# Kernel tuning notes

Hardware: AMD Instinct MI355X
Metric: run time of the kernel (lower is better)

## Reference

```python
import jax, jax.numpy as jnp
import numpy as np

# Model constants (match init_kwargs config)
D_MODEL, D_INNER, D_HEAD, N_HEADS = 1024, 2048, 64, 32
D_STATE, D_CONV, CHUNK, N_LAYERS = 64, 4, 256, 2
CONV_DIM = D_INNER + 2 * D_STATE        # n_groups = 1
D_IN_PROJ = 2 * D_INNER + 2 * D_STATE + N_HEADS
B_SZ, L_SEQ = 2, 4096
EPS = 1e-5


def setup_inputs() -> dict:
    key = jax.random.key(0)
    ks = jax.random.split(key, 8)
    x = jax.random.normal(ks[0], (B_SZ, L_SEQ, D_MODEL), jnp.float32)
    in_proj_w = jax.random.normal(ks[1], (N_LAYERS, D_IN_PROJ, D_MODEL), jnp.float32) * 0.02
    conv_w = jax.random.normal(ks[2], (N_LAYERS, CONV_DIM, D_CONV), jnp.float32) * 0.2
    conv_b = jax.random.normal(ks[3], (N_LAYERS, CONV_DIM), jnp.float32) * 0.02
    # dt_bias init as in the torch code: inverse-softplus of dt ~ LogUniform(1e-3, 1e-1)
    dt = jnp.exp(jax.random.uniform(ks[4], (N_LAYERS, N_HEADS))
                 * (np.log(0.1) - np.log(0.001)) + np.log(0.001))
    dt = jnp.clip(dt, 1e-4, None)
    dt_bias = dt + jnp.log(-jnp.expm1(-dt))
    A_log = jnp.log(jax.random.uniform(ks[5], (N_LAYERS, N_HEADS), minval=1.0, maxval=16.0))
    D = jnp.ones((N_LAYERS, N_HEADS), jnp.float32)
    gnorm_w = jnp.ones((N_LAYERS, D_INNER), jnp.float32)
    out_proj_w = jax.random.normal(ks[6], (N_LAYERS, D_MODEL, D_INNER), jnp.float32) * 0.02
    norm_w = jnp.ones((N_LAYERS, D_MODEL), jnp.float32)
    return dict(x=x, in_proj_w=in_proj_w, conv_w=conv_w, conv_b=conv_b, dt_bias=dt_bias,
                A_log=A_log, D=D, gnorm_w=gnorm_w, out_proj_w=out_proj_w, norm_w=norm_w)


def _rmsnorm(x, w, eps=EPS):
    return x * jax.lax.rsqrt(jnp.mean(x * x, axis=-1, keepdims=True) + eps) * w


def _segsum(x):
    # x: (..., T) -> (..., T, T) with S[i, j] = sum_{j < k <= i} x[k], -inf above diag
    T = x.shape[-1]
    cs = jnp.cumsum(x, axis=-1)
    d = cs[..., :, None] - cs[..., None, :]
    return jnp.where(jnp.tril(jnp.ones((T, T), bool)), d, -jnp.inf)


def _causal_conv1d(x, w, b):
    # depthwise causal conv: x (B,L,C), w (C,K), b (C)
    K = w.shape[-1]
    L = x.shape[1]
    xp = jnp.pad(x, ((0, 0), (K - 1, 0), (0, 0)))
    out = jnp.broadcast_to(b, x.shape)
    for i in range(K):
        out = out + xp[:, i:i + L, :] * w[:, i]
    return out


def _ssd(X, dt, A, B, C, D):
    # Exact chunked SSD scan (mamba_chunk_scan_combined), n_groups=1.
    # X (b,l,h,p), dt (b,l,h), A (h), B,C (b,l,n)
    b, l, h, p = X.shape
    n = B.shape[-1]
    nc = l // CHUNK
    Xdt = X * dt[..., None]
    dA = (dt * A).reshape(b, nc, CHUNK, h).transpose(0, 3, 1, 2)     # (b,h,z,c)
    dAcs = jnp.cumsum(dA, axis=-1)
    Lmat = jnp.exp(_segsum(dA))                                      # (b,h,z,c,c)
    Bc = B.reshape(b, nc, CHUNK, n)
    Cc = C.reshape(b, nc, CHUNK, n)
    Xc = Xdt.reshape(b, nc, CHUNK, h, p)
    # intra-chunk (diagonal) part
    G = jnp.einsum('bzln,bzsn->bzls', Cc, Bc)                        # (b,z,c,c)
    M = G[:, None] * Lmat                                            # (b,h,z,c,c)
    Yd = jnp.einsum('bhzls,bzshp->bzlhp', M, Xc)
    # chunk states
    decay_states = jnp.exp(dAcs[..., -1:] - dAcs)                    # (b,h,z,c)
    states = jnp.einsum('bzln,bhzl,bzlhp->bzhpn', Bc, decay_states, Xc)
    # inter-chunk recurrence
    chunk_decay = jnp.exp(_segsum(jnp.pad(dAcs[..., -1], ((0, 0), (0, 0), (1, 0)))))
    states0 = jnp.concatenate([jnp.zeros_like(states[:, :1]), states], axis=1)
    prev = jnp.einsum('bhzc,bchpn->bzhpn', chunk_decay, states0)[:, :-1]
    Yo = jnp.einsum('bzln,bzhpn,bhzl->bzlhp', Cc, prev, jnp.exp(dAcs))
    Y = (Yd + Yo).reshape(b, l, h, p) + X * D[None, None, :, None]
    return Y


def _block(x, in_w, cw, cb, dtb, a_log, d_skip, gw, ow, nw):
    b, l, _ = x.shape
    h = _rmsnorm(x, nw)
    zxbcdt = jnp.einsum('bld,ed->ble', h, in_w)
    z = zxbcdt[..., :D_INNER]
    xBC = zxbcdt[..., D_INNER:D_INNER + CONV_DIM]
    dt = jax.nn.softplus(zxbcdt[..., D_INNER + CONV_DIM:] + dtb)      # (b,l,H)
    xBC = jax.nn.silu(_causal_conv1d(xBC, cw, cb))
    xs = xBC[..., :D_INNER].reshape(b, l, N_HEADS, D_HEAD)
    Bm = xBC[..., D_INNER:D_INNER + D_STATE]
    Cm = xBC[..., D_INNER + D_STATE:]
    A = -jnp.exp(a_log)
    y = _ssd(xs, dt, A, Bm, Cm, d_skip).reshape(b, l, D_INNER)
    y = _rmsnorm(y * jax.nn.silu(z), gw)                              # gated RMSNorm (gate before norm)
    return x + jnp.einsum('bli,di->bld', y, ow)


def reference(x, in_proj_w, conv_w, conv_b, dt_bias, A_log, D, gnorm_w, out_proj_w, norm_w):
    for i in range(in_proj_w.shape[0]):
        x = _block(x, in_proj_w[i], conv_w[i], conv_b[i], dt_bias[i],
                   A_log[i], D[i], gnorm_w[i], out_proj_w[i], norm_w[i])
    return x
```

## Files before the change

### kernel.cpp

```cpp
#include <hip/hip_runtime.h>

#define DMODEL   1024
#define DINNER   2048
#define NHEADS   32
#define DHEAD    64
#define DSTATE   64
#define CONVDIM  2176
#define DINPROJ  4256
#define LSEQ     4096
#define BSZ      2
#define NCHUNK   16
#define CHUNK    256
#define NROWS    8192
#define NPAD     4352
#define XT_P     264
#define M_P      40

typedef __attribute__((ext_vector_type(8))) short  short8;
typedef __attribute__((ext_vector_type(4))) float  f32x4;
typedef __attribute__((ext_vector_type(4))) unsigned short us4;

__device__ __forceinline__ float bf2f(unsigned short u){
  return __uint_as_float(((unsigned int)u) << 16);
}
__device__ __forceinline__ unsigned short f2bf(float f){
  unsigned int i = __float_as_uint(f);
  i += 0x7fffu + ((i >> 16) & 1u);
  return (unsigned short)(i >> 16);
}

__device__ __forceinline__ void gl_lds16(const void* g, void* l){
  __builtin_amdgcn_global_load_lds(
      (const __attribute__((address_space(1))) unsigned int*)g,
      (__attribute__((address_space(3))) unsigned int*)l, 16, 0, 0);
}

__global__ void cast_pad_kernel(const float* __restrict__ src, unsigned short* __restrict__ dst,
                                int rows_src, int cols, long long total){
  long long i = (long long)blockIdx.x * 256 + threadIdx.x;
  if (i >= total) return;
  long long r = i / cols;
  dst[i] = (r < rows_src) ? f2bf(src[i]) : (unsigned short)0;
}

__global__ void rmsnorm_kernel(const float* __restrict__ x, const float* __restrict__ w,
                               unsigned short* __restrict__ out){
  int r = blockIdx.x, t = threadIdx.x;
  const float* xr = x + (size_t)r * DMODEL;
  float v[4]; float s = 0.f;
#pragma unroll
  for (int i = 0; i < 4; ++i){ v[i] = xr[t + i*256]; s += v[i]*v[i]; }
  __shared__ float red[4];
  for (int off = 32; off; off >>= 1) s += __shfl_down(s, off, 64);
  if ((t & 63) == 0) red[t >> 6] = s;
  __syncthreads();
  s = red[0] + red[1] + red[2] + red[3];
  float sc = rsqrtf(s * (1.f/DMODEL) + 1e-5f);
#pragma unroll
  for (int i = 0; i < 4; ++i)
    out[(size_t)r*DMODEL + t + i*256] = f2bf(v[i]*sc*w[t + i*256]);
}

template<int EPI>
__launch_bounds__(256, 3)
__global__ void gemm_bt(const unsigned short* __restrict__ A, const unsigned short* __restrict__ Bw,
                        void* __restrict__ Cout, const float* __restrict__ Cres,
                        int K, int Nstore){
  __shared__ __align__(16) unsigned short As[128*64];
  __shared__ __align__(16) unsigned short Bs[128*64];
  const int m0 = blockIdx.y * 128, n0 = blockIdx.x * 128;
  const int t = threadIdx.x, w = t >> 6, lane = t & 63;
  const int wr = w >> 1, wc = w & 1;
  const int srow = lane >> 3;
  const int scol = (lane & 7) * 8;
  f32x4 acc[4][4] = {};

  for (int k0 = 0; k0 < K; k0 += 64){
#pragma unroll
    for (int it = 0; it < 4; ++it){
      int rr = (w*4 + it)*8 + srow;
      gl_lds16(A  + (size_t)(m0 + rr)*K + k0 + scol, &As[(w*4 + it)*512]);
      gl_lds16(Bw + (size_t)(n0 + rr)*K + k0 + scol, &Bs[(w*4 + it)*512]);
    }
    __syncthreads();
#pragma unroll
    for (int kk = 0; kk < 64; kk += 32){
      short8 af[4], bfr[4];
      int col = kk + (lane >> 4)*8;
#pragma unroll
      for (int m = 0; m < 4; ++m)
        af[m] = *(const short8*)&As[(wr*64 + m*16 + (lane & 15))*64 + col];
#pragma unroll
      for (int n = 0; n < 4; ++n)
        bfr[n] = *(const short8*)&Bs[(wc*64 + n*16 + (lane & 15))*64 + col];
#pragma unroll
      for (int m = 0; m < 4; ++m)
#pragma unroll
        for (int n = 0; n < 4; ++n)
          acc[m][n] = __builtin_amdgcn_mfma_f32_16x16x32_bf16(af[m], bfr[n], acc[m][n], 0, 0, 0);
    }
    __syncthreads();
  }

#pragma unroll
  for (int m = 0; m < 4; ++m){
#pragma unroll
    for (int n = 0; n < 4; ++n){
      int col = n0 + wc*64 + n*16 + (lane & 15);
      if (col < Nstore){
#pragma unroll
        for (int r = 0; r < 4; ++r){
          int row = m0 + wr*64 + m*16 + (lane >> 4)*4 + r;
          if (EPI == 0)
            ((unsigned short*)Cout)[(size_t)row*Nstore + col] = f2bf(acc[m][n][r]);
          else
            ((float*)Cout)[(size_t)row*Nstore + col] =
                Cres[(size_t)row*Nstore + col] + acc[m][n][r];
        }
      }
    }
  }
}

__global__ void conv_silu_kernel(const unsigned short* __restrict__ zx,
                                 const float* __restrict__ cw, const float* __restrict__ cb,
                                 unsigned short* __restrict__ X, unsigned short* __restrict__ Bm,
                                 unsigned short* __restrict__ Cm){
  int gid = blockIdx.x*256 + threadIdx.x;
  if (gid >= (CONVDIM/8)*(NROWS/64)) return;
  const int oc = gid % (CONVDIM/8);
  const int rb = gid / (CONVDIM/8);
  const int c = oc*8;
  const size_t r0 = (size_t)rb*64;
  const int l0 = (int)(r0 & (LSEQ-1));
  float w[4][8], bias[8];
#pragma unroll
  for (int j = 0; j < 8; ++j){
    bias[j] = cb[c+j];
#pragma unroll
    for (int i = 0; i < 4; ++i) w[i][j] = cw[(c+j)*4 + i];
  }
  const unsigned short* src = zx + DINNER + c;
  float p[3][8];
#pragma unroll
  for (int i = 0; i < 3; ++i){
    if (l0 - 3 + i >= 0){
      short8 v = *(const short8*)(src + (r0 - 3 + i)*DINPROJ);
#pragma unroll
      for (int j = 0; j < 8; ++j) p[i][j] = bf2f((unsigned short)v[j]);
    } else {
#pragma unroll
      for (int j = 0; j < 8; ++j) p[i][j] = 0.f;
    }
  }
  for (int it = 0; it < 64; ++it){
    const size_t r = r0 + it;
    short8 v = *(const short8*)(src + r*DINPROJ);
    float cur[8];
    short8 ov;
#pragma unroll
    for (int j = 0; j < 8; ++j){
      cur[j] = bf2f((unsigned short)v[j]);
      float a = bias[j] + w[0][j]*p[0][j] + w[1][j]*p[1][j] + w[2][j]*p[2][j] + w[3][j]*cur[j];
      float s = a / (1.f + __expf(-a));
      ov[j] = (short)f2bf(s);
    }
    if (c < DINNER)             *(short8*)(X  + r*DINNER + c) = ov;
    else if (c < DINNER+DSTATE) *(short8*)(Bm + r*DSTATE + (c-DINNER)) = ov;
    else                        *(short8*)(Cm + r*DSTATE + (c-DINNER-DSTATE)) = ov;
#pragma unroll
    for (int j = 0; j < 8; ++j){ p[0][j]=p[1][j]; p[1][j]=p[2][j]; p[2][j]=cur[j]; }
  }
}

__global__ void dtscan_kernel(const unsigned short* __restrict__ zx, const float* __restrict__ dtb,
                              const float* __restrict__ A_log,
                              float* __restrict__ dt_sp, float* __restrict__ dAcs_g){
  const int z = blockIdx.x, hh = blockIdx.y, b = blockIdx.z;
  const int t = threadIdx.x;
  __shared__ float sdA[CHUNK];
  const float Ah = -__expf(A_log[hh]);
  size_t r = (size_t)b*LSEQ + z*CHUNK + t;
  float raw = bf2f(zx[r*DINPROJ + DINNER + CONVDIM + hh]) + dtb[hh];
  float dtv = raw > 20.f ? raw : log1pf(__expf(raw));
  sdA[t] = dtv * Ah;
  __syncthreads();
  for (int off = 1; off < CHUNK; off <<= 1){
    float v = (t >= off) ? sdA[t - off] : 0.f;
    __syncthreads();
    sdA[t] += v;
    __syncthreads();
  }
  size_t hb = (size_t)(b*NHEADS + hh);
  dt_sp[hb*LSEQ + z*CHUNK + t] = dtv;
  dAcs_g[(hb*NCHUNK + z)*CHUNK + t] = sdA[t];
}

__launch_bounds__(256, 2)
__global__ void chunk_main_kernel(const unsigned short* __restrict__ X,
                                  const unsigned short* __restrict__ Bm,
                                  const unsigned short* __restrict__ Cm,
                                  const float* __restrict__ dt_sp,
                                  const float* __restrict__ dAcs_g,
                                  float* __restrict__ states,
                                  unsigned short* __restrict__ Yb){
  const int z = blockIdx.x, hh = blockIdx.y, b = blockIdx.z;
  const int t = threadIdx.x, w = t >> 6, lane = t & 63;
  __shared__ __align__(16) unsigned short Xt[64 * XT_P];
  __shared__ __align__(16) unsigned short U[64 * XT_P];
  __shared__ float sdA[CHUNK];
  __shared__ float sdt[CHUNK];

  const size_t row0 = (size_t)b*LSEQ + z*CHUNK;
  const size_t hb = (size_t)(b*NHEADS + hh);
  sdA[t] = dAcs_g[(hb*NCHUNK + z)*CHUNK + t];
  sdt[t] = dt_sp[hb*LSEQ + z*CHUNK + t];
  __syncthreads();
  const float total = sdA[CHUNK-1];

  for (int it = 0; it < 16; ++it){
    int l = it*16 + (t >> 4);
    int p4 = (t & 15) * 4;
    float dtl = sdt[l];
    float dec = __expf(total - sdA[l]);
    us4 xv = *(const us4*)(X  + (row0 + l)*DINNER + hh*DHEAD + p4);
    us4 bv = *(const us4*)(Bm + (row0 + l)*DSTATE + p4);
#pragma unroll
    for (int j = 0; j < 4; ++j){
      Xt[(p4 + j)*XT_P + l] = f2bf(bf2f(xv[j]) * dtl);
      U [(p4 + j)*XT_P + l] = f2bf(bf2f(bv[j]) * dec);
    }
  }
  __syncthreads();

  {
    f32x4 sacc[4] = {};
    for (int k2 = 0; k2 < 8; ++k2){
      int kc = k2*32 + (lane >> 4)*8;
      short8 a = *(const short8*)&U[(w*16 + (lane & 15))*XT_P + kc];
#pragma unroll
      for (int pt = 0; pt < 4; ++pt){
        short8 bfr = *(const short8*)&Xt[(pt*16 + (lane & 15))*XT_P + kc];
        sacc[pt] = __builtin_amdgcn_mfma_f32_16x16x32_bf16(a, bfr, sacc[pt], 0, 0, 0);
      }
    }
    float* sp = states + (((size_t)b*NCHUNK + z)*NHEADS + hh)*(DHEAD*DSTATE);
#pragma unroll
    for (int pt = 0; pt < 4; ++pt){
      int p = pt*16 + (lane & 15);
#pragma unroll
      for (int r = 0; r < 4; ++r){
        int n = w*16 + (lane >> 4)*4 + r;
        sp[p*DSTATE + n] = sacc[pt][r];
      }
    }
  }
  __syncthreads();

  unsigned short* Mw = U + w * (64 * M_P);
  short8 cfr[4][2];
#pragma unroll
  for (int lt = 0; lt < 4; ++lt){
    int lg = w + lt*4;
#pragma unroll
    for (int k2 = 0; k2 < 2; ++k2)
      cfr[lt][k2] = *(const short8*)(Cm + (row0 + lg*16 + (lane & 15))*DSTATE + k2*32 + (lane >> 4)*8);
  }
  f32x4 yacc[4][4] = {};
  for (int st = 0; st < 8; ++st){
    short8 gb[2][2];
#pragma unroll
    for (int ss = 0; ss < 2; ++ss)
#pragma unroll
      for (int k2 = 0; k2 < 2; ++k2)
        gb[ss][k2] = *(const short8*)(Bm + (row0 + st*32 + ss*16 + (lane & 15))*DSTATE + k2*32 + (lane >> 4)*8);
    short8 xb[4];
#pragma unroll
    for (int pt = 0; pt < 4; ++pt)
      xb[pt] = *(const short8*)&Xt[(pt*16 + (lane & 15))*XT_P + st*32 + (lane >> 4)*8];
#pragma unroll
    for (int lt = 0; lt < 4; ++lt){
      int lg = w + lt*4;
      if (st*32 > lg*16 + 15) continue;
#pragma unroll
      for (int ss = 0; ss < 2; ++ss){
        f32x4 g = {};
        g = __builtin_amdgcn_mfma_f32_16x16x32_bf16(cfr[lt][0], gb[ss][0], g, 0, 0, 0);
        g = __builtin_amdgcn_mfma_f32_16x16x32_bf16(cfr[lt][1], gb[ss][1], g, 0, 0, 0);
        int s = st*32 + ss*16 + (lane & 15);
        float sdAs = sdA[s];
#pragma unroll
        for (int r = 0; r < 4; ++r){
          int l = lg*16 + (lane >> 4)*4 + r;
          float m = (s <= l) ? __expf(sdA[l] - sdAs) : 0.f;
          Mw[(lt*16 + (lane >> 4)*4 + r)*M_P + ss*16 + (lane & 15)] = f2bf(g[r] * m);
        }
      }
      short8 mf = *(const short8*)&Mw[(lt*16 + (lane & 15))*M_P + (lane >> 4)*8];
#pragma unroll
      for (int pt = 0; pt < 4; ++pt)
        yacc[lt][pt] = __builtin_amdgcn_mfma_f32_16x16x32_bf16(mf, xb[pt], yacc[lt][pt], 0, 0, 0);
    }
  }
  __syncthreads();

  unsigned short* Yst = U + w * 4096;
#pragma unroll
  for (int lt = 0; lt < 4; ++lt)
#pragma unroll
    for (int pt = 0; pt < 4; ++pt)
#pragma unroll
      for (int r = 0; r < 4; ++r){
        int row = lt*16 + (lane >> 4)*4 + r;
        int c = pt*16 + (lane & 15);
        int cs = (c & 7) | ((((c >> 3) ^ (row & 7)) & 7) << 3);
        Yst[row*64 + cs] = f2bf(yacc[lt][pt][r]);
      }
  __syncthreads();
  {
    int ltl = lane >> 4, rr = lane & 15;
    int row = ltl*16 + rr;
    int lg = (w + ltl*4)*16 + rr;
    unsigned short* dst = Yb + (row0 + lg)*DINNER + hh*DHEAD;
#pragma unroll
    for (int k = 0; k < 8; ++k){
      short8 v = *(const short8*)&Yst[row*64 + ((k ^ (row & 7)) << 3)];
      *(short8*)(dst + k*8) = v;
    }
  }
}

__launch_bounds__(256)
__global__ void state_recur_kernel(const float* __restrict__ states, const float* __restrict__ dAcs_g,
                                   unsigned short* __restrict__ prev_bf){
  const int hh = blockIdx.x, b = blockIdx.y, t = threadIdx.x;
  float S[16];
#pragma unroll
  for (int k = 0; k < 16; ++k) S[k] = 0.f;
  for (int z = 0; z < NCHUNK; ++z){
    size_t base = (((size_t)b*NCHUNK + z)*NHEADS + hh)*(DHEAD*DSTATE);
    float cd = __expf(dAcs_g[(((size_t)(b*NHEADS + hh))*NCHUNK + z)*CHUNK + CHUNK-1]);
#pragma unroll
    for (int k = 0; k < 16; ++k){
      size_t idx = base + (size_t)k*256 + t;
      float st = states[idx];
      prev_bf[idx] = f2bf(S[k]);
      S[k] = S[k]*cd + st;
    }
  }
}

__launch_bounds__(256, 4)
__global__ void chunk_out_kernel(const unsigned short* __restrict__ X,
                                 const unsigned short* __restrict__ Cm,
                                 const float* __restrict__ dAcs_g, const unsigned short* __restrict__ prev_bf,
                                 const float* __restrict__ Dp, unsigned short* __restrict__ Yb){
  const int z = blockIdx.x, hh = blockIdx.y, b = blockIdx.z;
  const int t = threadIdx.x, w = t >> 6, lane = t & 63;
  __shared__ __align__(16) unsigned short Yo[4][64*64];
  __shared__ float sdA[CHUNK];
  const size_t row0 = (size_t)b*LSEQ + z*CHUNK;
  sdA[t] = dAcs_g[(((size_t)(b*NHEADS + hh))*NCHUNK + z)*CHUNK + t];
  __syncthreads();
  const unsigned short* pvb = prev_bf + (((size_t)b*NCHUNK + z)*NHEADS + hh)*(DHEAD*DSTATE);
  const float Dh = Dp[hh];

  f32x4 acc[4][4] = {};
#pragma unroll
  for (int k2 = 0; k2 < 2; ++k2){
    int kc = k2*32 + (lane >> 4)*8;
    short8 a[4], bfr[4];
#pragma unroll
    for (int lt = 0; lt < 4; ++lt)
      a[lt] = *(const short8*)(Cm + (row0 + w*64 + lt*16 + (lane & 15))*DSTATE + kc);
#pragma unroll
    for (int pt = 0; pt < 4; ++pt)
      bfr[pt] = *(const short8*)(pvb + (size_t)(pt*16 + (lane & 15))*DSTATE + kc);
#pragma unroll
    for (int lt = 0; lt < 4; ++lt)
#pragma unroll
      for (int pt = 0; pt < 4; ++pt)
        acc[lt][pt] = __builtin_amdgcn_mfma_f32_16x16x32_bf16(a[lt], bfr[pt], acc[lt][pt], 0, 0, 0);
  }

#pragma unroll
  for (int lt = 0; lt < 4; ++lt){
    float eA[4];
#pragma unroll
    for (int r = 0; r < 4; ++r)
      eA[r] = __expf(sdA[w*64 + lt*16 + (lane >> 4)*4 + r]);
#pragma unroll
    for (int pt = 0; pt < 4; ++pt){
      int c = pt*16 + (lane & 15);
#pragma unroll
      for (int r = 0; r < 4; ++r){
        int row = lt*16 + (lane >> 4)*4 + r;
        int blk = ((c >> 2) ^ (row & 15)) & 15;
        Yo[w][row*64 + (c & 3) + (blk << 2)] = f2bf(acc[lt][pt][r] * eA[r]);
      }
    }
  }
  __syncthreads();
  {
    int l = w*64 + lane;
    const unsigned short* xr = X + (row0 + l)*DINNER + hh*DHEAD;
    unsigned short* yr = Yb + (row0 + l)*DINNER + hh*DHEAD;
#pragma unroll
    for (int k = 0; k < 16; ++k){
      us4 v = *(const us4*)&Yo[w][lane*64 + (((k ^ (lane & 15)) & 15) << 2)];
      us4 yb = *(const us4*)(yr + k*4);
      us4 xv = *(const us4*)(xr + k*4);
      us4 o;
#pragma unroll
      for (int j = 0; j < 4; ++j)
        o[j] = f2bf(bf2f(yb[j]) + bf2f(v[j]) + Dh*bf2f(xv[j]));
      *(us4*)(yr + k*4) = o;
    }
  }
}

__global__ void gated_rmsnorm_kernel(const unsigned short* __restrict__ Yb,
                                     const unsigned short* __restrict__ zx,
                                     const float* __restrict__ gw, unsigned short* __restrict__ out){
  int r = blockIdx.x, t = threadIdx.x;
  float vals[8]; float s = 0.f;
#pragma unroll
  for (int i = 0; i < 8; ++i){
    int c = t + i*256;
    float y  = bf2f(Yb[(size_t)r*DINNER + c]);
    float zv = bf2f(zx[(size_t)r*DINPROJ + c]);
    float g  = y * (zv / (1.f + __expf(-zv)));
    vals[i] = g; s += g*g;
  }
  __shared__ float red[4];
  for (int off = 32; off; off >>= 1) s += __shfl_down(s, off, 64);
  if ((t & 63) == 0) red[t >> 6] = s;
  __syncthreads();
  s = red[0] + red[1] + red[2] + red[3];
  float sc = rsqrtf(s * (1.f/DINNER) + 1e-5f);
#pragma unroll
  for (int i = 0; i < 8; ++i)
    out[(size_t)r*DINNER + t + i*256] = f2bf(vals[i]*sc*gw[t + i*256]);
}

extern "C" void kernel_launch(void* const* d_in, const int* in_sizes, int n_in,
                              void* d_out, int out_size, void* d_ws, size_t ws_size,
                              hipStream_t stream){
  const float* x      = (const float*)d_in[0];
  const float* in_w   = (const float*)d_in[1];
  const float* conv_w = (const float*)d_in[2];
  const float* conv_b = (const float*)d_in[3];
  const float* dt_b   = (const float*)d_in[4];
  const float* A_log  = (const float*)d_in[5];
  const float* Dp     = (const float*)d_in[6];
  const float* gnw    = (const float*)d_in[7];
  const float* out_w  = (const float*)d_in[8];
  const float* norm_w = (const float*)d_in[9];
  float* outp = (float*)d_out;

  const size_t NEEDED =
      (size_t)NROWS*DMODEL*2 + (size_t)NPAD*DMODEL*2 + (size_t)DMODEL*DINNER*2
    + (size_t)NROWS*DINPROJ*2 + (size_t)NROWS*DINNER*2  + (size_t)NROWS*DINNER*2
    + (size_t)NROWS*DSTATE*2*2 + (size_t)BSZ*NHEADS*LSEQ*4
    + (size_t)BSZ*NHEADS*NCHUNK*CHUNK*4
    + (size_t)BSZ*NCHUNK*NHEADS*DHEAD*DSTATE*4
    + (size_t)BSZ*NCHUNK*NHEADS*DHEAD*DSTATE*2
    + 40*256;
  if (ws_size < NEEDED) return;

  char* p = (char*)d_ws;
  auto alloc = [&](size_t n){ char* r = p; p += (n + 255) & ~(size_t)255; return (void*)r; };
  unsigned short* h    = (unsigned short*)alloc((size_t)NROWS*DMODEL*2);
  unsigned short* wA   = (unsigned short*)alloc((size_t)NPAD*DMODEL*2);
  unsigned short* wO   = (unsigned short*)alloc((size_t)DMODEL*DINNER*2);
  unsigned short* zx   = (unsigned short*)alloc((size_t)NROWS*DINPROJ*2);
  unsigned short* X    = (unsigned short*)alloc((size_t)NROWS*DINNER*2);
  unsigned short* Yb   = (unsigned short*)alloc((size_t)NROWS*DINNER*2);
  unsigned short* Bm   = (unsigned short*)alloc((size_t)NROWS*DSTATE*2);
  unsigned short* Cm   = (unsigned short*)alloc((size_t)NROWS*DSTATE*2);
  float* dtbuf  = (float*)alloc((size_t)BSZ*NHEADS*LSEQ*4);
  float* dAcs   = (float*)alloc((size_t)BSZ*NHEADS*NCHUNK*CHUNK*4);
  float* states = (float*)alloc((size_t)BSZ*NCHUNK*NHEADS*DHEAD*DSTATE*4);
  unsigned short* prev_bf = (unsigned short*)alloc((size_t)BSZ*NCHUNK*NHEADS*DHEAD*DSTATE*2);
  unsigned short* yn = X;

  for (int layer = 0; layer < 2; ++layer){
    const float* xprev = (layer == 0) ? x : outp;
    float* xnext = outp;

    cast_pad_kernel<<<(NPAD*DMODEL + 255)/256, 256, 0, stream>>>(
        in_w + (size_t)layer*DINPROJ*DMODEL, wA, DINPROJ, DMODEL, (long long)NPAD*DMODEL);
    rmsnorm_kernel<<<NROWS, 256, 0, stream>>>(xprev, norm_w + layer*DMODEL, h);
    gemm_bt<0><<<dim3(NPAD/128, NROWS/128), 256, 0, stream>>>(
        h, wA, (void*)zx, nullptr, DMODEL, DINPROJ);
    conv_silu_kernel<<<((CONVDIM/8)*(NROWS/64) + 255)/256, 256, 0, stream>>>(
        zx, conv_w + (size_t)layer*CONVDIM*4, conv_b + layer*CONVDIM, X, Bm, Cm);
    dtscan_kernel<<<dim3(NCHUNK, NHEADS, BSZ), 256, 0, stream>>>(
        zx, dt_b + layer*NHEADS, A_log + layer*NHEADS, dtbuf, dAcs);
    chunk_main_kernel<<<dim3(NCHUNK, NHEADS, BSZ), 256, 0, stream>>>(
        X, Bm, Cm, dtbuf, dAcs, states, Yb);
    state_recur_kernel<<<dim3(NHEADS, BSZ), 256, 0, stream>>>(states, dAcs, prev_bf);
    chunk_out_kernel<<<dim3(NCHUNK, NHEADS, BSZ), 256, 0, stream>>>(
        X, Cm, dAcs, prev_bf, Dp + layer*NHEADS, Yb);
    gated_rmsnorm_kernel<<<NROWS, 256, 0, stream>>>(Yb, zx, gnw + layer*DINNER, yn);
    cast_pad_kernel<<<(DMODEL*DINNER + 255)/256, 256, 0, stream>>>(
        out_w + (size_t)layer*DMODEL*DINNER, wO, DMODEL, DINNER, (long long)DMODEL*DINNER);
    gemm_bt<1><<<dim3(DMODEL/128, NROWS/128), 256, 0, stream>>>(
        yn, wO, (void*)xnext, xprev, DINNER, DMODEL);
  }
  (void)in_sizes; (void)n_in; (void)out_size;
}
```

Before: 732.6 us.

## Fuse chunk output with gated RMSNorm and remap GEMM blocks across XCDs

Merges the chunk-output kernel (C·prev state MFMA plus D skip) with the gated RMSNorm into one kernel. Each 512-thread block handles 16 rows across all heads, so the Yb intermediate is no longer written and read back, and one launch is removed. The GEMMs now use a 1D grid with an XCD-aware remap of block IDs, meant to improve L2 locality across the chiplets. In exchange, the fused kernel uses about 66KB of LDS per block and reloads prev_bf per 16-row slice, which increases redundant state reads.

```diff
diff --git a/kernel.cpp b/kernel.cpp
--- a/kernel.cpp
+++ b/kernel.cpp
@@ -65,10 +65,13 @@
 __launch_bounds__(256, 3)
 __global__ void gemm_bt(const unsigned short* __restrict__ A, const unsigned short* __restrict__ Bw,
                         void* __restrict__ Cout, const float* __restrict__ Cres,
-                        int K, int Nstore){
+                        int K, int Nstore, int nbx){
   __shared__ __align__(16) unsigned short As[128*64];
   __shared__ __align__(16) unsigned short Bs[128*64];
-  const int m0 = blockIdx.y * 128, n0 = blockIdx.x * 128;
+  int id = blockIdx.x;
+  const int nwg = gridDim.x;
+  if ((nwg & 7) == 0) id = (id & 7)*(nwg >> 3) + (id >> 3);
+  const int m0 = (id / nbx) * 128, n0 = (id % nbx) * 128;
   const int t = threadIdx.x, w = t >> 6, lane = t & 63;
   const int wr = w >> 1, wc = w & 1;
   const int srow = lane >> 3;
@@ -350,97 +353,103 @@
   }
 }
 
-__launch_bounds__(256, 4)
-__global__ void chunk_out_kernel(const unsigned short* __restrict__ X,
+__launch_bounds__(512, 2)
+__global__ void chunk_fin_kernel(const unsigned short* __restrict__ X,
                                  const unsigned short* __restrict__ Cm,
-                                 const float* __restrict__ dAcs_g, const unsigned short* __restrict__ prev_bf,
-                                 const float* __restrict__ Dp, unsigned short* __restrict__ Yb){
-  const int z = blockIdx.x, hh = blockIdx.y, b = blockIdx.z;
+                                 const unsigned short* __restrict__ zx,
+                                 const float* __restrict__ dAcs_g,
+                                 const unsigned short* __restrict__ prev_bf,
+                                 const float* __restrict__ Dp,
+                                 const unsigned short* __restrict__ Yb,
+                                 const float* __restrict__ gnw,
+                                 unsigned short* __restrict__ yn){
+  const int s = blockIdx.x;
+  const int b = blockIdx.y;
+  const int z = s >> 4, sl = s & 15;
   const int t = threadIdx.x, w = t >> 6, lane = t & 63;
-  __shared__ __align__(16) unsigned short Yo[4][64*64];
-  __shared__ float sdA[CHUNK];
-  const size_t row0 = (size_t)b*LSEQ + z*CHUNK;
-  sdA[t] = dAcs_g[(((size_t)(b*NHEADS + hh))*NCHUNK + z)*CHUNK + t];
-  __syncthreads();
-  const unsigned short* pvb = prev_bf + (((size_t)b*NCHUNK + z)*NHEADS + hh)*(DHEAD*DSTATE);
-  const float Dh = Dp[hh];
-
-  f32x4 acc[4][4] = {};
-#pragma unroll
-  for (int k2 = 0; k2 < 2; ++k2){
-    int kc = k2*32 + (lane >> 4)*8;
-    short8 a[4], bfr[4];
-#pragma unroll
-    for (int lt = 0; lt < 4; ++lt)
-      a[lt] = *(const short8*)(Cm + (row0 + w*64 + lt*16 + (lane & 15))*DSTATE + kc);
-#pragma unroll
-    for (int pt = 0; pt < 4; ++pt)
-      bfr[pt] = *(const short8*)(pvb + (size_t)(pt*16 + (lane & 15))*DSTATE + kc);
-#pragma unroll
-    for (int lt = 0; lt < 4; ++lt)
-#pragma unroll
-      for (int pt = 0; pt < 4; ++pt)
-        acc[lt][pt] = __builtin_amdgcn_mfma_f32_16x16x32_bf16(a[lt], bfr[pt], acc[lt][pt], 0, 0, 0);
-  }
-
-#pragma unroll
-  for (int lt = 0; lt < 4; ++lt){
-    float eA[4];
-#pragma unroll
-    for (int r = 0; r < 4; ++r)
-      eA[r] = __expf(sdA[w*64 + lt*16 + (lane >> 4)*4 + r]);
+  const size_t row0 = (size_t)b*LSEQ + z*CHUNK + sl*16;
+  __shared__ __align__(16) unsigned short Yg[16][2056];
+  __shared__ float seA[NHEADS][16];
+  __shared__ float sDp[NHEADS];
+
+  {
+    int hh = t >> 4, r = t & 15;
+    seA[hh][r] = __expf(dAcs_g[(((size_t)(b*NHEADS + hh))*NCHUNK + z)*CHUNK + sl*16 + r]);
+    if (t < NHEADS) sDp[t] = Dp[t];
+  }
+  __syncthreads();
+
+  short8 cf[2];
+#pragma unroll
+  for (int k2 = 0; k2 < 2; ++k2)
+    cf[k2] = *(const short8*)(Cm + (row0 + (lane & 15))*DSTATE + k2*32 + (lane >> 4)*8);
+
+  for (int hi = 0; hi < 4; ++hi){
+    int hh = w*4 + hi;
+    const unsigned short* pvb = prev_bf + (((size_t)b*NCHUNK + z)*NHEADS + hh)*(DHEAD*DSTATE);
+    f32x4 acc[4] = {};
+#pragma unroll
+    for (int k2 = 0; k2 < 2; ++k2){
+      int kc = k2*32 + (lane >> 4)*8;
+#pragma unroll
+      for (int pt = 0; pt < 4; ++pt){
+        short8 bv = *(const short8*)(pvb + (size_t)(pt*16 + (lane & 15))*DSTATE + kc);
+        acc[pt] = __builtin_amdgcn_mfma_f32_16x16x32_bf16(cf[k2], bv, acc[pt], 0, 0, 0);
+      }
+    }
 #pragma unroll
     for (int pt = 0; pt < 4; ++pt){
-      int c = pt*16 + (lane & 15);
+      int c = hh*DHEAD + pt*16 + (lane & 15);
 #pragma unroll
       for (int r = 0; r < 4; ++r){
-        int row = lt*16 + (lane >> 4)*4 + r;
-        int blk = ((c >> 2) ^ (row & 15)) & 15;
-        Yo[w][row*64 + (c & 3) + (blk << 2)] = f2bf(acc[lt][pt][r] * eA[r]);
-      }
-    }
-  }
-  __syncthreads();
-  {
-    int l = w*64 + lane;
-    const unsigned short* xr = X + (row0 + l)*DINNER + hh*DHEAD;
-    unsigned short* yr = Yb + (row0 + l)*DINNER + hh*DHEAD;
-#pragma unroll
-    for (int k = 0; k < 16; ++k){
-      us4 v = *(const us4*)&Yo[w][lane*64 + (((k ^ (lane & 15)) & 15) << 2)];
-      us4 yb = *(const us4*)(yr + k*4);
-      us4 xv = *(const us4*)(xr + k*4);
-      us4 o;
-#pragma unroll
-      for (int j = 0; j < 4; ++j)
-        o[j] = f2bf(bf2f(yb[j]) + bf2f(v[j]) + Dh*bf2f(xv[j]));
-      *(us4*)(yr + k*4) = o;
-    }
-  }
-}
-
-__global__ void gated_rmsnorm_kernel(const unsigned short* __restrict__ Yb,
-                                     const unsigned short* __restrict__ zx,
-                                     const float* __restrict__ gw, unsigned short* __restrict__ out){
-  int r = blockIdx.x, t = threadIdx.x;
-  float vals[8]; float s = 0.f;
-#pragma unroll
-  for (int i = 0; i < 8; ++i){
-    int c = t + i*256;
-    float y  = bf2f(Yb[(size_t)r*DINNER + c]);
-    float zv = bf2f(zx[(size_t)r*DINPROJ + c]);
-    float g  = y * (zv / (1.f + __expf(-zv)));
-    vals[i] = g; s += g*g;
-  }
-  __shared__ float red[4];
-  for (int off = 32; off; off >>= 1) s += __shfl_down(s, off, 64);
-  if ((t & 63) == 0) red[t >> 6] = s;
-  __syncthreads();
-  s = red[0] + red[1] + red[2] + red[3];
-  float sc = rsqrtf(s * (1.f/DINNER) + 1e-5f);
-#pragma unroll
-  for (int i = 0; i < 8; ++i)
-    out[(size_t)r*DINNER + t + i*256] = f2bf(vals[i]*sc*gw[t + i*256]);
+        int row = (lane >> 4)*4 + r;
+        Yg[row][c] = f2bf(acc[pt][r] * seA[hh][row]);
+      }
+    }
+  }
+  __syncthreads();
+
+  const int row = t >> 5, i = t & 31;
+  const size_t grow = row0 + row;
+  float ss = 0.f;
+#pragma unroll
+  for (int j = 0; j < 8; ++j){
+    int c0 = i*8 + j*256;
+    short8 yo = *(const short8*)&Yg[row][c0];
+    short8 yd = *(const short8*)(Yb + grow*DINNER + c0);
+    short8 xv = *(const short8*)(X  + grow*DINNER + c0);
+    short8 zv = *(const short8*)(zx + grow*DINPROJ + c0);
+    float Dh = sDp[c0 >> 6];
+    short8 og;
+#pragma unroll
+    for (int q = 0; q < 8; ++q){
+      float y = bf2f((unsigned short)yd[q]) + bf2f((unsigned short)yo[q])
+              + Dh*bf2f((unsigned short)xv[q]);
+      float zf = bf2f((unsigned short)zv[q]);
+      float g = y * (zf / (1.f + __expf(-zf)));
+      ss += g*g;
+      og[q] = (short)f2bf(g);
+    }
+    *(short8*)&Yg[row][c0] = og;
+  }
+  for (int off = 16; off; off >>= 1) ss += __shfl_down(ss, off, 32);
+  float sc = __shfl(ss, 0, 32);
+  sc = rsqrtf(sc * (1.f/DINNER) + 1e-5f);
+  __syncthreads();
+
+#pragma unroll
+  for (int j = 0; j < 8; ++j){
+    int c0 = i*8 + j*256;
+    short8 g = *(const short8*)&Yg[row][c0];
+    f32x4 w0 = *(const f32x4*)(gnw + c0);
+    f32x4 w1 = *(const f32x4*)(gnw + c0 + 4);
+    short8 o;
+#pragma unroll
+    for (int q = 0; q < 4; ++q) o[q]   = (short)f2bf(bf2f((unsigned short)g[q])  *sc*w0[q]);
+#pragma unroll
+    for (int q = 0; q < 4; ++q) o[q+4] = (short)f2bf(bf2f((unsigned short)g[q+4])*sc*w1[q]);
+    *(short8*)(yn + grow*DINNER + c0) = o;
+  }
 }
 
 extern "C" void kernel_launch(void* const* d_in, const int* in_sizes, int n_in,
@@ -491,8 +500,8 @@
     cast_pad_kernel<<<(NPAD*DMODEL + 255)/256, 256, 0, stream>>>(
         in_w + (size_t)layer*DINPROJ*DMODEL, wA, DINPROJ, DMODEL, (long long)NPAD*DMODEL);
     rmsnorm_kernel<<<NROWS, 256, 0, stream>>>(xprev, norm_w + layer*DMODEL, h);
-    gemm_bt<0><<<dim3(NPAD/128, NROWS/128), 256, 0, stream>>>(
-        h, wA, (void*)zx, nullptr, DMODEL, DINPROJ);
+    gemm_bt<0><<<dim3((NPAD/128)*(NROWS/128)), 256, 0, stream>>>(
+        h, wA, (void*)zx, nullptr, DMODEL, DINPROJ, NPAD/128);
     conv_silu_kernel<<<((CONVDIM/8)*(NROWS/64) + 255)/256, 256, 0, stream>>>(
         zx, conv_w + (size_t)layer*CONVDIM*4, conv_b + layer*CONVDIM, X, Bm, Cm);
     dtscan_kernel<<<dim3(NCHUNK, NHEADS, BSZ), 256, 0, stream>>>(
@@ -500,13 +509,12 @@
     chunk_main_kernel<<<dim3(NCHUNK, NHEADS, BSZ), 256, 0, stream>>>(
         X, Bm, Cm, dtbuf, dAcs, states, Yb);
     state_recur_kernel<<<dim3(NHEADS, BSZ), 256, 0, stream>>>(states, dAcs, prev_bf);
-    chunk_out_kernel<<<dim3(NCHUNK, NHEADS, BSZ), 256, 0, stream>>>(
-        X, Cm, dAcs, prev_bf, Dp + layer*NHEADS, Yb);
-    gated_rmsnorm_kernel<<<NROWS, 256, 0, stream>>>(Yb, zx, gnw + layer*DINNER, yn);
+    chunk_fin_kernel<<<dim3(256, BSZ), 512, 0, stream>>>(
+        X, Cm, zx, dAcs, prev_bf, Dp + layer*NHEADS, Yb, gnw + (size_t)layer*DINNER, yn);
     cast_pad_kernel<<<(DMODEL*DINNER + 255)/256, 256, 0, stream>>>(
         out_w + (size_t)layer*DMODEL*DINNER, wO, DMODEL, DINNER, (long long)DMODEL*DINNER);
-    gemm_bt<1><<<dim3(DMODEL/128, NROWS/128), 256, 0, stream>>>(
-        yn, wO, (void*)xnext, xprev, DINNER, DMODEL);
+    gemm_bt<1><<<dim3((DMODEL/128)*(NROWS/128)), 256, 0, stream>>>(
+        yn, wO, (void*)xnext, xprev, DINNER, DMODEL, DMODEL/128);
   }
   (void)in_sizes; (void)n_in; (void)out_size;
 }
```

New measurement: 696.7 us. 4.9% less time.
